# Optimization experiments

Measured on AMD Instinct MI355X. Metric: run time of the kernel, lower is better.

The kernel has to match this reference:

```python
import jax, jax.numpy as jnp
import numpy as np

B, S, D, H = 2, 2048, 1024, 16
HD = D // H  # 64


def setup_inputs() -> dict:
    key = jax.random.key(0)
    ks = jax.random.split(key, 10)
    inp = {
        "queries": jax.random.normal(ks[0], (B, S, D), dtype=jnp.float32),
        "keys": jax.random.normal(ks[1], (B, S, D), dtype=jnp.float32),
        "values": jax.random.normal(ks[2], (B, S, D), dtype=jnp.float32),
        "attention_mask": jax.random.randint(ks[3], (B, S), 0, 2, dtype=jnp.int32),
        # Linear params (torch nn.Linear: y = x @ W.T + b), scaled like default init
        "Wq": jax.random.normal(ks[4], (D, D), dtype=jnp.float32) / np.sqrt(D),
        "bq": jnp.zeros((D,), dtype=jnp.float32),
        "Wk": jax.random.normal(ks[5], (D, D), dtype=jnp.float32) / np.sqrt(D),
        "bk": jnp.zeros((D,), dtype=jnp.float32),
        "Wv": jax.random.normal(ks[6], (D, D), dtype=jnp.float32) / np.sqrt(D),
        "bv": jnp.zeros((D,), dtype=jnp.float32),
    }
    return inp


def _split_heads(x):
    # torch.chunk along last dim + stack(dim=1) == reshape + transpose
    b, s, d = x.shape
    return x.reshape(b, s, H, HD).transpose(0, 2, 1, 3)  # [B,H,S,hd]


def reference(queries, keys, values, attention_mask, Wq, bq, Wk, bk, Wv, bv):
    q = jax.nn.relu(queries @ Wq.T + bq)
    k = jax.nn.relu(keys @ Wk.T + bk)
    v = jax.nn.relu(values @ Wv.T + bv)
    qh, kh, vh = _split_heads(q), _split_heads(k), _split_heads(v)
    score = jnp.einsum("bhqd,bhkd->bhqk", qh, kh) / jnp.sqrt(jnp.float32(HD))
    # enc mask: [B,1,S,1] broadcast over key dim — masks whole query rows where mask==0
    row_mask = (attention_mask == 0)[:, None, :, None]
    score = jnp.where(row_mask, jnp.float32(-1e9), score)
    attn = jax.nn.softmax(score, axis=-1)
    a = jnp.einsum("bhqk,bhkd->bhqd", attn, vh)  # [B,H,S,hd]
    # faithful to original: permute(0,1,3,2) then reshape to (B,S,D)
    a = a.transpose(0, 1, 3, 2).reshape(q.shape[0], q.shape[1], q.shape[2])
    return a + queries
```

## Files before the change

kernel.cpp:

```cpp
#include <hip/hip_runtime.h>
#include <hip/hip_bf16.h>

#define DEV __device__ __forceinline__

typedef __attribute__((ext_vector_type(8))) short short8;
typedef __attribute__((ext_vector_type(4))) float f32x4;

#define MFMA16(a, b, c) __builtin_amdgcn_mfma_f32_16x16x32_bf16((a), (b), (c), 0, 0, 0)

static constexpr int B_ = 2, S_ = 2048, D_ = 1024, H_ = 16, HD_ = 64;
static constexpr long NX = (long)B_ * S_ * D_;
static constexpr long NW = (long)D_ * D_;

DEV short f2bf(float f) {
    __hip_bfloat16 h = __float2bfloat16(f);
    union { __hip_bfloat16 hh; short s; } u;
    u.hh = h;
    return u.s;
}

DEV float bf2f(short s) {
    union { float f; unsigned u; } x;
    x.u = ((unsigned)(unsigned short)s) << 16;
    return x.f;
}

DEV unsigned cvtpk(float a, float b) {
    unsigned r;
    asm("v_cvt_pk_bf16_f32 %0, %1, %2" : "=v"(r) : "v"(a), "v"(b));
    return r;
}

DEV short8 ld8(const short* p) { return *(const short8*)p; }

DEV void gld16(const short* g, short* l) {
    __builtin_amdgcn_global_load_lds(
        (const __attribute__((address_space(1))) unsigned int*)g,
        (__attribute__((address_space(3))) unsigned int*)l, 16, 0, 0);
}

__global__ __launch_bounds__(256) void convert_all(
    const float* __restrict__ q, const float* __restrict__ k, const float* __restrict__ v,
    const float* __restrict__ wq, const float* __restrict__ wk, const float* __restrict__ wv,
    short* __restrict__ qb, short* __restrict__ kb, short* __restrict__ vb,
    short* __restrict__ wqb, short* __restrict__ wkb, short* __restrict__ wvb) {
    long tid = (long)blockIdx.x * 256 + threadIdx.x;
    long e = tid * 4;
    const float* src; short* dst; long off;
    if      (e < NX)            { src = q;  dst = qb;  off = e; }
    else if (e < 2*NX)          { src = k;  dst = kb;  off = e - NX; }
    else if (e < 3*NX)          { src = v;  dst = vb;  off = e - 2*NX; }
    else if (e < 3*NX + NW)     { src = wq; dst = wqb; off = e - 3*NX; }
    else if (e < 3*NX + 2*NW)   { src = wk; dst = wkb; off = e - 3*NX - NW; }
    else                        { src = wv; dst = wvb; off = e - 3*NX - 2*NW; }
    float4 f = *(const float4*)(src + off);
    short4 o;
    o.x = f2bf(f.x); o.y = f2bf(f.y); o.z = f2bf(f.z); o.w = f2bf(f.w);
    *(short4*)(dst + off) = o;
}

__global__ __launch_bounds__(256) void gemm_bias_relu(
    const short* __restrict__ X0, const short* __restrict__ X1, const short* __restrict__ X2,
    const short* __restrict__ W0, const short* __restrict__ W1, const short* __restrict__ W2,
    const float* __restrict__ b0, const float* __restrict__ b1, const float* __restrict__ b2,
    short* __restrict__ O0, short* __restrict__ O1, short* __restrict__ O2) {
    __shared__ short As[2][128 * 32];
    __shared__ short Bs[2][128 * 32];

    const int z = blockIdx.z;
    const short* X   = (z == 0) ? X0 : (z == 1) ? X1 : X2;
    const short* W   = (z == 0) ? W0 : (z == 1) ? W1 : W2;
    const float* bia = (z == 0) ? b0 : (z == 1) ? b1 : b2;
    short*       Out = (z == 0) ? O0 : (z == 1) ? O1 : O2;

    const int tid  = threadIdx.x;
    const int wid  = tid >> 6;
    const int lane = tid & 63;
    const int id   = lane & 15;
    const int quad = lane >> 4;
    const int m0 = blockIdx.y * 128;
    const int n0 = blockIdx.x * 128;
    const int wm = (wid >> 1) * 64;
    const int wn = (wid & 1) * 64;

    const short* Ag0 = X + (long)(m0 + wid * 32 + (lane >> 2)) * D_ + (lane & 3) * 8;
    const short* Bg0 = W + (long)(n0 + wid * 32 + (lane >> 2)) * D_ + (lane & 3) * 8;
    const int offW = wid * 1024;

    f32x4 acc[4][4] = {};

    gld16(Ag0,            &As[0][offW]);
    gld16(Ag0 + 16 * D_,  &As[0][offW + 512]);
    gld16(Bg0,            &Bs[0][offW]);
    gld16(Bg0 + 16 * D_,  &Bs[0][offW + 512]);

    for (int kk = 0; kk < D_; kk += 32) {
        const int cur = (kk >> 5) & 1;
        __syncthreads();
        if (kk + 32 < D_) {
            const int nxt = cur ^ 1;
            gld16(Ag0 + kk + 32,            &As[nxt][offW]);
            gld16(Ag0 + 16 * D_ + kk + 32,  &As[nxt][offW + 512]);
            gld16(Bg0 + kk + 32,            &Bs[nxt][offW]);
            gld16(Bg0 + 16 * D_ + kk + 32,  &Bs[nxt][offW + 512]);
        }

        short8 af[4], bf[4];
#pragma unroll
        for (int i = 0; i < 4; i++) af[i] = ld8(&As[cur][(wm + 16*i + id) * 32 + quad * 8]);
#pragma unroll
        for (int j = 0; j < 4; j++) bf[j] = ld8(&Bs[cur][(wn + 16*j + id) * 32 + quad * 8]);
#pragma unroll
        for (int i = 0; i < 4; i++)
#pragma unroll
            for (int j = 0; j < 4; j++)
                acc[i][j] = MFMA16(af[i], bf[j], acc[i][j]);
    }

#pragma unroll
    for (int j = 0; j < 4; j++) {
        int col = n0 + wn + 16*j + id;
        float bj = bia[col];
#pragma unroll
        for (int i = 0; i < 4; i++) {
#pragma unroll
            for (int r = 0; r < 4; r++) {
                int row = m0 + wm + 16*i + quad*4 + r;
                float val = fmaxf(acc[i][j][r] + bj, 0.f);
                Out[(long)row * D_ + col] = f2bf(val);
            }
        }
    }
}

__global__ __launch_bounds__(256) void transpose_v(const short* __restrict__ Vp,
                                                   short* __restrict__ VT) {
    __shared__ short tile[64 * 64];
    const int bh = blockIdx.y;
    const int b = bh >> 4, h = bh & 15;
    const int s0 = blockIdx.x * 64;
    const int t = threadIdx.x;
#pragma unroll
    for (int it = 0; it < 2; it++) {
        int row = (t >> 3) + 32 * it;
        int u   = t & 7;
        short8 d = ld8(Vp + (long)(b * S_ + s0 + row) * D_ + h * HD_ + u * 8);
        *(short8*)(&tile[row * 64 + (u ^ ((row >> 3) & 7)) * 8]) = d;
    }
    __syncthreads();
#pragma unroll
    for (int it = 0; it < 2; it++) {
        int e  = (t >> 3) + 32 * it;
        int sb = (t & 7) * 8;
        short8 o;
#pragma unroll
        for (int u = 0; u < 8; u++) {
            int row = sb + u;
            o[u] = tile[row * 64 + (((e >> 3) ^ ((row >> 3) & 7)) * 8) + (e & 7)];
        }
        *(short8*)(VT + ((long)bh * HD_ + e) * S_ + s0 + sb) = o;
    }
}

__global__ __launch_bounds__(256, 2) void attention(
    const short* __restrict__ Qb, const short* __restrict__ Kb,
    const short* __restrict__ VT, const int* __restrict__ mask,
    const float* __restrict__ queries, float* __restrict__ out) {
    __shared__ short Ks[2][64 * 64];
    __shared__ short Vs[2][64 * 64];
    __shared__ short pl[4][2 * 16 * 72];

    const int tid  = threadIdx.x;
    const int wid  = tid >> 6;
    const int lane = tid & 63;
    const int id   = lane & 15;
    const int quad = lane >> 4;

    const int bid = blockIdx.x;
    const int w   = bid >> 3;
    const int bh  = (bid & 7) + 8 * (w & 3);
    const int qt  = w >> 2;
    const int b   = bh >> 4;
    const int h   = bh & 15;
    const int q0  = qt * 128 + wid * 32;

    short8 qf[2][2];
#pragma unroll
    for (int g = 0; g < 2; g++) {
        const short* qbase = Qb + (long)(b * S_ + q0 + g * 16 + id) * D_ + h * HD_ + quad * 8;
        short8 f0 = ld8(qbase);
        short8 f1 = ld8(qbase + 32);
        const float qsc = mask[b * S_ + q0 + g * 16 + id] ? 0.125f : 0.f;
#pragma unroll
        for (int i = 0; i < 8; i++) {
            f0[i] = f2bf(bf2f(f0[i]) * qsc);
            f1[i] = f2bf(bf2f(f1[i]) * qsc);
        }
        qf[g][0] = f0; qf[g][1] = f1;
    }

    const int srow = wid * 16 + (lane >> 3);
    const int su   = (lane & 7) ^ (srow & 7);
    const short* kg0 = Kb + ((long)b * S_ + srow) * D_ + h * HD_ + su * 8;
    const short* vg0 = VT + (((long)(b * H_ + h) * HD_) + srow) * S_ + su * 8;
    short* plw = pl[wid];

    const int swz = id & 7;

    float l4[2][4] = {};
    f32x4 o[2][4] = {};

    gld16(kg0,            &Ks[0][wid * 1024]);
    gld16(kg0 + 8 * D_,   &Ks[0][wid * 1024 + 512]);
    gld16(vg0,            &Vs[0][wid * 1024]);
    gld16(vg0 + 8 * S_,   &Vs[0][wid * 1024 + 512]);

    for (int c0 = 0; c0 < S_; c0 += 64) {
        const int cur = (c0 >> 6) & 1;
        __syncthreads();
        if (c0 + 64 < S_) {
            const int nxt = cur ^ 1;
            const long cg = (long)(c0 + 64);
            gld16(kg0 + cg * D_,           &Ks[nxt][wid * 1024]);
            gld16(kg0 + cg * D_ + 8 * D_,  &Ks[nxt][wid * 1024 + 512]);
            gld16(vg0 + cg,                &Vs[nxt][wid * 1024]);
            gld16(vg0 + cg + 8 * S_,       &Vs[nxt][wid * 1024 + 512]);
        }

        f32x4 s[2][4];
#pragma unroll
        for (int g = 0; g < 2; g++)
#pragma unroll
            for (int t = 0; t < 4; t++) s[g][t] = (f32x4){0.f, 0.f, 0.f, 0.f};
#pragma unroll
        for (int t = 0; t < 4; t++) {
            short8 a0 = ld8(&Ks[cur][(16*t + id) * 64 + ((quad    ) ^ swz) * 8]);
            short8 a1 = ld8(&Ks[cur][(16*t + id) * 64 + ((quad ^ 4) ^ swz) * 8]);
            s[0][t] = MFMA16(a0, qf[0][0], s[0][t]);
            s[0][t] = MFMA16(a1, qf[0][1], s[0][t]);
            s[1][t] = MFMA16(a0, qf[1][0], s[1][t]);
            s[1][t] = MFMA16(a1, qf[1][1], s[1][t]);
        }

#pragma unroll
        for (int g = 0; g < 2; g++) {
            short* plg = plw + g * (16 * 72);
#pragma unroll
            for (int t = 0; t < 4; t++) {
                float p0 = __expf(s[g][t][0]);
                float p1 = __expf(s[g][t][1]);
                float p2 = __expf(s[g][t][2]);
                float p3 = __expf(s[g][t][3]);
                l4[g][0] += p0; l4[g][1] += p1; l4[g][2] += p2; l4[g][3] += p3;
                uint2 w2;
                w2.x = cvtpk(p0, p1);
                w2.y = cvtpk(p2, p3);
                *(uint2*)(&plg[id * 72 + 16 * t + quad * 4]) = w2;
            }
        }
        short8 pf[2][2];
#pragma unroll
        for (int g = 0; g < 2; g++) {
            short* plg = plw + g * (16 * 72);
            pf[g][0] = ld8(&plg[id * 72 + quad * 8]);
            pf[g][1] = ld8(&plg[id * 72 + 32 + quad * 8]);
        }

#pragma unroll
        for (int j2 = 0; j2 < 4; j2++) {
#pragma unroll
            for (int kh = 0; kh < 2; kh++) {
                short8 va = ld8(&Vs[cur][(16*j2 + id) * 64 + (((kh << 2) + quad) ^ swz) * 8]);
                o[0][j2] = MFMA16(va, pf[0][kh], o[0][j2]);
                o[1][j2] = MFMA16(va, pf[1][kh], o[1][j2]);
            }
        }
    }

    const long obase = (long)b * (S_ * D_) + (long)h * (HD_ * S_);
#pragma unroll
    for (int g = 0; g < 2; g++) {
        float l = l4[g][0] + l4[g][1] + l4[g][2] + l4[g][3];
        l += __shfl_xor(l, 16);
        l += __shfl_xor(l, 32);
        const float linv = 1.f / l;
#pragma unroll
        for (int j2 = 0; j2 < 4; j2++) {
#pragma unroll
            for (int r = 0; r < 4; r++) {
                int dim = 16 * j2 + quad * 4 + r;
                long idx = obase + (long)dim * S_ + q0 + g * 16 + id;
                out[idx] = o[g][j2][r] * linv + queries[idx];
            }
        }
    }
}

extern "C" void kernel_launch(void* const* d_in, const int* in_sizes, int n_in,
                              void* d_out, int out_size, void* d_ws, size_t ws_size,
                              hipStream_t stream) {
    const float* queries = (const float*)d_in[0];
    const float* keys    = (const float*)d_in[1];
    const float* values  = (const float*)d_in[2];
    const int*   mask    = (const int*)d_in[3];
    const float* Wq = (const float*)d_in[4];
    const float* bq = (const float*)d_in[5];
    const float* Wk = (const float*)d_in[6];
    const float* bk = (const float*)d_in[7];
    const float* Wv = (const float*)d_in[8];
    const float* bv = (const float*)d_in[9];
    float* out = (float*)d_out;

    short* ws  = (short*)d_ws;
    short* qb  = ws;
    short* kb  = qb  + NX;
    short* vb  = kb  + NX;
    short* wqb = vb  + NX;
    short* wkb = wqb + NW;
    short* wvb = wkb + NW;
    short* Q   = wvb + NW;
    short* K   = Q   + NX;
    short* Vp  = K   + NX;
    short* VT  = Vp  + NX;

    convert_all<<<15360, 256, 0, stream>>>(queries, keys, values, Wq, Wk, Wv,
                                           qb, kb, vb, wqb, wkb, wvb);
    gemm_bias_relu<<<dim3(8, 32, 3), 256, 0, stream>>>(qb, kb, vb, wqb, wkb, wvb,
                                                       bq, bk, bv, Q, K, Vp);
    transpose_v<<<dim3(32, 32), 256, 0, stream>>>(Vp, VT);
    attention<<<512, 256, 0, stream>>>(Q, K, VT, mask, queries, out);
}
```

Before: 200.8 us.

## Software-pipeline attention: deeper K/V prefetch and PV matmul lagged one tile

The attention loop now keeps three K buffers and four V buffers in shared memory and prefetches two tiles ahead. Explicit vmcnt waits replace the full __syncthreads. The P·V MFMA for tile i-1 is issued after the QK^T MFMAs of tile i, so the exp/pack work and LDS round-trip of one tile can overlap with matrix ops of the other. This aims to hide global-load latency and the softmax-to-PV dependency stall. The cost is more LDS per block, which may reduce occupancy, and a reliance on hand-tuned waitcnt counts.

Result: no change. 203.5 us (+1.3%).

```diff
diff --git a/kernel.cpp b/kernel.cpp
--- a/kernel.cpp
+++ b/kernel.cpp
@@ -166,8 +166,8 @@
     const short* __restrict__ Qb, const short* __restrict__ Kb,
     const short* __restrict__ VT, const int* __restrict__ mask,
     const float* __restrict__ queries, float* __restrict__ out) {
-    __shared__ short Ks[2][64 * 64];
-    __shared__ short Vs[2][64 * 64];
+    __shared__ short Ks[3][64 * 64];
+    __shared__ short Vs[4][64 * 64];
     __shared__ short pl[4][2 * 16 * 72];
 
     const int tid  = threadIdx.x;
@@ -184,6 +184,25 @@
     const int h   = bh & 15;
     const int q0  = qt * 128 + wid * 32;
 
+    const int srow = wid * 16 + (lane >> 3);
+    const int su   = (lane & 7) ^ (srow & 7);
+    const short* kg0 = Kb + ((long)b * S_ + srow) * D_ + h * HD_ + su * 8;
+    const short* vg0 = VT + (((long)(b * H_ + h) * HD_) + srow) * S_ + su * 8;
+    short* plw = pl[wid];
+    const int swz = id & 7;
+
+#define STAGE_ATT(c, kb_, vb_)                                          \
+    do {                                                                \
+        const long cg = (long)(c) * 64;                                 \
+        gld16(kg0 + cg * D_,          &Ks[(kb_)][wid * 1024]);          \
+        gld16(kg0 + cg * D_ + 8 * D_, &Ks[(kb_)][wid * 1024 + 512]);    \
+        gld16(vg0 + cg,               &Vs[(vb_)][wid * 1024]);          \
+        gld16(vg0 + cg + 8 * S_,      &Vs[(vb_)][wid * 1024 + 512]);    \
+    } while (0)
+
+    STAGE_ATT(0, 0, 0);
+    STAGE_ATT(1, 1, 1);
+
     short8 qf[2][2];
 #pragma unroll
     for (int g = 0; g < 2; g++) {
@@ -199,34 +218,19 @@
         qf[g][0] = f0; qf[g][1] = f1;
     }
 
-    const int srow = wid * 16 + (lane >> 3);
-    const int su   = (lane & 7) ^ (srow & 7);
-    const short* kg0 = Kb + ((long)b * S_ + srow) * D_ + h * HD_ + su * 8;
-    const short* vg0 = VT + (((long)(b * H_ + h) * HD_) + srow) * S_ + su * 8;
-    short* plw = pl[wid];
-
-    const int swz = id & 7;
-
     float l4[2][4] = {};
     f32x4 o[2][4] = {};
-
-    gld16(kg0,            &Ks[0][wid * 1024]);
-    gld16(kg0 + 8 * D_,   &Ks[0][wid * 1024 + 512]);
-    gld16(vg0,            &Vs[0][wid * 1024]);
-    gld16(vg0 + 8 * S_,   &Vs[0][wid * 1024 + 512]);
-
-    for (int c0 = 0; c0 < S_; c0 += 64) {
-        const int cur = (c0 >> 6) & 1;
-        __syncthreads();
-        if (c0 + 64 < S_) {
-            const int nxt = cur ^ 1;
-            const long cg = (long)(c0 + 64);
-            gld16(kg0 + cg * D_,           &Ks[nxt][wid * 1024]);
-            gld16(kg0 + cg * D_ + 8 * D_,  &Ks[nxt][wid * 1024 + 512]);
-            gld16(vg0 + cg,                &Vs[nxt][wid * 1024]);
-            gld16(vg0 + cg + 8 * S_,       &Vs[nxt][wid * 1024 + 512]);
-        }
-
+    short8 pfp[2][2];
+
+    for (int i = 0; i < 32; ++i) {
+        if (i < 31) asm volatile("s_waitcnt vmcnt(4) lgkmcnt(0)" ::: "memory");
+        else        asm volatile("s_waitcnt vmcnt(0) lgkmcnt(0)" ::: "memory");
+        __builtin_amdgcn_s_barrier();
+        __builtin_amdgcn_sched_barrier(0);
+
+        if (i + 2 < 32) STAGE_ATT(i + 2, (i + 2) % 3, (i + 2) & 3);
+
+        const short* Kc = &Ks[i % 3][0];
         f32x4 s[2][4];
 #pragma unroll
         for (int g = 0; g < 2; g++)
@@ -234,12 +238,25 @@
             for (int t = 0; t < 4; t++) s[g][t] = (f32x4){0.f, 0.f, 0.f, 0.f};
 #pragma unroll
         for (int t = 0; t < 4; t++) {
-            short8 a0 = ld8(&Ks[cur][(16*t + id) * 64 + ((quad    ) ^ swz) * 8]);
-            short8 a1 = ld8(&Ks[cur][(16*t + id) * 64 + ((quad ^ 4) ^ swz) * 8]);
+            short8 a0 = ld8(&Kc[(16*t + id) * 64 + ((quad    ) ^ swz) * 8]);
+            short8 a1 = ld8(&Kc[(16*t + id) * 64 + ((quad ^ 4) ^ swz) * 8]);
             s[0][t] = MFMA16(a0, qf[0][0], s[0][t]);
             s[0][t] = MFMA16(a1, qf[0][1], s[0][t]);
             s[1][t] = MFMA16(a0, qf[1][0], s[1][t]);
             s[1][t] = MFMA16(a1, qf[1][1], s[1][t]);
+        }
+
+        if (i > 0) {
+            const short* Vc = &Vs[(i - 1) & 3][0];
+#pragma unroll
+            for (int j2 = 0; j2 < 4; j2++) {
+#pragma unroll
+                for (int kh = 0; kh < 2; kh++) {
+                    short8 va = ld8(&Vc[(16*j2 + id) * 64 + (((kh << 2) + quad) ^ swz) * 8]);
+                    o[0][j2] = MFMA16(va, pfp[0][kh], o[0][j2]);
+                    o[1][j2] = MFMA16(va, pfp[1][kh], o[1][j2]);
+                }
+            }
         }
 
 #pragma unroll
@@ -258,24 +275,27 @@
                 *(uint2*)(&plg[id * 72 + 16 * t + quad * 4]) = w2;
             }
         }
-        short8 pf[2][2];
 #pragma unroll
         for (int g = 0; g < 2; g++) {
             short* plg = plw + g * (16 * 72);
-            pf[g][0] = ld8(&plg[id * 72 + quad * 8]);
-            pf[g][1] = ld8(&plg[id * 72 + 32 + quad * 8]);
-        }
-
+            pfp[g][0] = ld8(&plg[id * 72 + quad * 8]);
+            pfp[g][1] = ld8(&plg[id * 72 + 32 + quad * 8]);
+        }
+    }
+
+    {
+        const short* Vc = &Vs[31 & 3][0];
 #pragma unroll
         for (int j2 = 0; j2 < 4; j2++) {
 #pragma unroll
             for (int kh = 0; kh < 2; kh++) {
-                short8 va = ld8(&Vs[cur][(16*j2 + id) * 64 + (((kh << 2) + quad) ^ swz) * 8]);
-                o[0][j2] = MFMA16(va, pf[0][kh], o[0][j2]);
-                o[1][j2] = MFMA16(va, pf[1][kh], o[1][j2]);
-            }
-        }
-    }
+                short8 va = ld8(&Vc[(16*j2 + id) * 64 + (((kh << 2) + quad) ^ swz) * 8]);
+                o[0][j2] = MFMA16(va, pfp[0][kh], o[0][j2]);
+                o[1][j2] = MFMA16(va, pfp[1][kh], o[1][j2]);
+            }
+        }
+    }
+#undef STAGE_ATT
 
     const long obase = (long)b * (S_ * D_) + (long)h * (HD_ * S_);
 #pragma unroll
```
